# Optimization experiments

Measured on AMD Instinct MI355X. Metric: run time of the kernel, lower is better.

The kernel has to match this reference:

```python
import jax, jax.numpy as jnp
import numpy as np

NUM_USERS = 100000
NUM_ITEMS = 50000
N = NUM_USERS + NUM_ITEMS
E = 3000000
DIM = 64


def setup_inputs() -> dict:
    key = jax.random.key(0)
    ks = jax.random.split(key, 8)
    emb_users = 0.01 * jax.random.normal(ks[0], (NUM_USERS, DIM), dtype=jnp.float32)
    emb_items = 0.01 * jax.random.normal(ks[1], (NUM_ITEMS, DIM), dtype=jnp.float32)
    # GCNConv linear weights (bias separate, as in PyG: lin(bias=False) + bias param)
    s = 1.0 / np.sqrt(DIM)
    W1 = jax.random.uniform(ks[2], (DIM, DIM), jnp.float32, -s, s)
    b1 = jnp.zeros((DIM,), jnp.float32)
    W2 = jax.random.uniform(ks[3], (DIM, DIM), jnp.float32, -s, s)
    b2 = jnp.zeros((DIM,), jnp.float32)
    edge_index = jax.random.randint(ks[4], (2, E), 0, N, dtype=jnp.int64)
    edge_weight = jax.random.uniform(ks[5], (E,), jnp.float32)
    return {"emb_users": emb_users, "emb_items": emb_items,
            "W1": W1, "b1": b1, "W2": W2, "b2": b2,
            "edge_index": edge_index, "edge_weight": edge_weight}


def _gcn_conv(x, W, b, row, col):
    """PyG GCNConv with add_self_loops=True, improved=False, unit edge weights.
    out[i] = sum_{j->i} d_j^-1/2 d_i^-1/2 (x_j W) + d_i^-1 (x_i W) + b
    where d includes the self-loop (+1).
    """
    n = x.shape[0]
    xw = x @ W                                           # [N, D]
    deg = jax.ops.segment_sum(jnp.ones_like(row, dtype=x.dtype), col,
                              num_segments=n) + 1.0      # in-degree + self-loop
    dinv = jax.lax.rsqrt(deg)                            # [N]
    coef = dinv[row] * dinv[col]                         # [E]
    msg = xw[row] * coef[:, None]                        # gather + scale  [E, D]
    out = jax.ops.segment_sum(msg, col, num_segments=n)  # scatter-add     [N, D]
    out = out + xw * (dinv * dinv)[:, None]              # self-loop term
    return out + b


def reference(emb_users, emb_items, W1, b1, W2, b2, edge_index, edge_weight):
    # edge_weight is accepted by forward() but never passed to the GCN convs
    row, col = edge_index[0], edge_index[1]
    emb = jnp.concatenate([emb_users, emb_items], axis=0)  # [N, D]
    embs = [emb]
    for W, b in ((W1, b1), (W2, b2)):
        emb = _gcn_conv(emb, W, b, row, col)
        embs.append(emb)
        emb = jax.nn.relu(emb)
    return jnp.stack(embs)  # [num_layers+1, N, D]
```

## Files before the change

### kernel.cpp

```cpp
#include <hip/hip_runtime.h>
#include <hip/hip_fp16.h>

#define DIM 64
#define BPN 1024
#define ECHUNK 8192
#define MAXNB 160

typedef _Float16 f16x8 __attribute__((ext_vector_type(8)));
typedef float f32x4 __attribute__((ext_vector_type(4)));


__global__ __launch_bounds__(1024) void bucket_count_kernel(
    const int* __restrict__ col, int* __restrict__ bucket_cnt, int E, int NB) {
  __shared__ int h[MAXNB];
  for (int t = threadIdx.x; t < NB; t += blockDim.x) h[t] = 0;
  __syncthreads();
  int base = blockIdx.x * ECHUNK;
  int end = min(base + ECHUNK, E);
  for (int e = base + (int)threadIdx.x; e < end; e += blockDim.x)
    atomicAdd(&h[col[e] >> 10], 1);
  __syncthreads();
  for (int t = threadIdx.x; t < NB; t += blockDim.x)
    if (h[t]) atomicAdd(&bucket_cnt[t], h[t]);
}

__global__ void bucket_scan_kernel(const int* __restrict__ bucket_cnt,
                                   int* __restrict__ bucket_base,
                                   int* __restrict__ bucket_cursor,
                                   int* __restrict__ off, int NB, int N, int E) {
  if (threadIdx.x == 0) {
    int s = 0;
    for (int b = 0; b < NB; b++) { bucket_base[b] = s; bucket_cursor[b] = s; s += bucket_cnt[b]; }
    bucket_base[NB] = s;
    off[N] = E;
  }
}

__global__ __launch_bounds__(1024) void bucket_scatter_kernel(
    const int* __restrict__ row, const int* __restrict__ col,
    int* __restrict__ bucket_cursor, int* __restrict__ packed, int E, int NB) {
  __shared__ int h[MAXNB];
  __shared__ int excl0[MAXNB];
  __shared__ int cur[MAXNB];
  __shared__ int gbase[MAXNB];
  __shared__ int staging[ECHUNK];
  __shared__ unsigned short map[ECHUNK];
  const int tid = threadIdx.x;
  for (int t = tid; t < NB; t += blockDim.x) h[t] = 0;
  __syncthreads();
  int base = blockIdx.x * ECHUNK;
  int end = min(base + ECHUNK, E);
  int total = end - base;
  for (int e = base + tid; e < end; e += blockDim.x)
    atomicAdd(&h[col[e] >> 10], 1);
  __syncthreads();
  if (tid == 0) {
    int s = 0;
    for (int b = 0; b < NB; b++) { excl0[b] = s; cur[b] = s; s += h[b]; }
  }
  __syncthreads();
  if (tid < NB) {
    if (h[tid] > 0) gbase[tid] = atomicAdd(&bucket_cursor[tid], h[tid]);
    int s = excl0[tid], c = h[tid];
    for (int j = 0; j < c; j++) map[s + j] = (unsigned short)tid;
  }
  __syncthreads();
  for (int e = base + tid; e < end; e += blockDim.x) {
    int c = col[e];
    int b = c >> 10;
    int pos = atomicAdd(&cur[b], 1);
    staging[pos] = ((c & (BPN - 1)) << 18) | row[e];
  }
  __syncthreads();
  for (int idx = tid; idx < total; idx += blockDim.x) {
    int b = map[idx];
    packed[gbase[b] + idx - excl0[b]] = staging[idx];
  }
}

__global__ __launch_bounds__(1024) void bucket_csr_kernel(
    const int* __restrict__ packed, const int* __restrict__ bucket_base,
    int* __restrict__ perm_row, int* __restrict__ off, float* __restrict__ dinv, int N) {
  __shared__ int nh[BPN];
  __shared__ int ncur[BPN];
  __shared__ int wsum[16];
  __shared__ int woff[16];
  const int b = blockIdx.x;
  const int tid = threadIdx.x;
  const int ebase = bucket_base[b];
  const int cnt = bucket_base[b + 1] - ebase;
  nh[tid] = 0;
  __syncthreads();
  for (int i = tid; i < cnt; i += 1024)
    atomicAdd(&nh[packed[ebase + i] >> 18], 1);
  __syncthreads();
  const int lane = tid & 63, wid = tid >> 6;
  int v = nh[tid], x = v;
#pragma unroll
  for (int d = 1; d < 64; d <<= 1) {
    int t = __shfl_up(x, d, 64);
    if (lane >= d) x += t;
  }
  if (lane == 63) wsum[wid] = x;
  __syncthreads();
  if (tid == 0) {
    int s = 0;
#pragma unroll
    for (int k = 0; k < 16; k++) { woff[k] = s; s += wsum[k]; }
  }
  __syncthreads();
  int excl = woff[wid] + x - v;
  ncur[tid] = excl;
  int node = b * BPN + tid;
  if (node < N) {
    off[node] = ebase + excl;
    dinv[node] = rsqrtf((float)v + 1.0f);
  }
  __syncthreads();
  for (int i = tid; i < cnt; i += 1024) {
    int p = packed[ebase + i];
    int local = p >> 18;
    int pos = atomicAdd(&ncur[local], 1);
    perm_row[ebase + pos] = p & 0x3FFFF;
  }
}

__global__ __launch_bounds__(256) void xw_mfma_kernel(
    const float* __restrict__ xa, const float* __restrict__ xb,
    const float* __restrict__ W, float* __restrict__ out0,
    __half* __restrict__ xwh, int NU, int N, int do_relu) {
  __shared__ _Float16 Wt[64 * 72];
  for (int t = threadIdx.x; t < 4096; t += 256) {
    int k = t >> 6, n = t & 63;
    Wt[n * 72 + k] = (_Float16)W[t];
  }
  __syncthreads();
  const int lane = threadIdx.x & 63;
  const int wid = threadIdx.x >> 6;
  const int m = lane & 15;
  const int quad = lane >> 4;
  f16x8 bfrag[4][2];
#pragma unroll
  for (int c = 0; c < 4; c++)
#pragma unroll
    for (int s = 0; s < 2; s++)
      bfrag[c][s] = *(const f16x8*)&Wt[(c * 16 + m) * 72 + s * 32 + quad * 8];

  const int rbase = (blockIdx.x * 4 + wid) * 16;
  if (rbase >= N) return;
  const int r = rbase + m;
  const int rr = min(r, N - 1);
  const float* src = (xb == nullptr || rr < NU) ? xa + (size_t)rr * DIM
                                                : xb + (size_t)(rr - NU) * DIM;
  f16x8 afrag[2];
#pragma unroll
  for (int s = 0; s < 2; s++) {
    float4 u0 = *(const float4*)(src + s * 32 + quad * 8);
    float4 u1 = *(const float4*)(src + s * 32 + quad * 8 + 4);
    if (out0 != nullptr && r < N) {
      float4* o = (float4*)(out0 + (size_t)r * DIM);
      o[s * 8 + quad * 2] = u0;
      o[s * 8 + quad * 2 + 1] = u1;
    }
    if (do_relu) {
      u0.x = fmaxf(u0.x, 0.f); u0.y = fmaxf(u0.y, 0.f);
      u0.z = fmaxf(u0.z, 0.f); u0.w = fmaxf(u0.w, 0.f);
      u1.x = fmaxf(u1.x, 0.f); u1.y = fmaxf(u1.y, 0.f);
      u1.z = fmaxf(u1.z, 0.f); u1.w = fmaxf(u1.w, 0.f);
    }
    afrag[s][0] = (_Float16)u0.x; afrag[s][1] = (_Float16)u0.y;
    afrag[s][2] = (_Float16)u0.z; afrag[s][3] = (_Float16)u0.w;
    afrag[s][4] = (_Float16)u1.x; afrag[s][5] = (_Float16)u1.y;
    afrag[s][6] = (_Float16)u1.z; afrag[s][7] = (_Float16)u1.w;
  }
  f32x4 acc[4];
#pragma unroll
  for (int c = 0; c < 4; c++) {
    acc[c] = (f32x4){0.f, 0.f, 0.f, 0.f};
    acc[c] = __builtin_amdgcn_mfma_f32_16x16x32_f16(afrag[0], bfrag[c][0], acc[c], 0, 0, 0);
    acc[c] = __builtin_amdgcn_mfma_f32_16x16x32_f16(afrag[1], bfrag[c][1], acc[c], 0, 0, 0);
  }
#pragma unroll
  for (int reg = 0; reg < 4; reg++) {
    int orow = rbase + quad * 4 + reg;
    if (orow < N) {
      __half* dst = xwh + (size_t)orow * DIM + m;
#pragma unroll
      for (int c = 0; c < 4; c++)
        dst[c * 16] = __float2half(acc[c][reg]);
    }
  }
}

__global__ void aggregate_kernel(const __half* __restrict__ xwh, const int* __restrict__ off,
                                 const int* __restrict__ perm_row, const float* __restrict__ dinv,
                                 const float* __restrict__ b, float* __restrict__ out, int n) {
  const int lane = threadIdx.x & 63;
  const int i = blockIdx.x * (blockDim.x >> 6) + (threadIdx.x >> 6);
  if (i >= n) return;
  const int esel = lane >> 3;
  const int j = lane & 7;
  const float di = dinv[i];
  float acc[8];
#pragma unroll
  for (int q = 0; q < 8; q++) acc[q] = 0.0f;
  if (esel == 0) {
    float4 f = ((const float4*)xwh)[(size_t)i * 8 + j];
    const __half2* h = (const __half2*)&f;
    float w = di * di;
#pragma unroll
    for (int q = 0; q < 4; q++) {
      float2 p = __half22float2(h[q]);
      acc[2 * q] = p.x * w;
      acc[2 * q + 1] = p.y * w;
    }
  }
  int s0 = off[i], s1 = off[i + 1];
  for (int s = s0; s < s1; s += 64) {
    int m = s1 - s;
    if (m > 64) m = 64;
    int myr = 0;
    float myc = 0.0f;
    if (lane < m) {
      myr = perm_row[s + lane];
      myc = dinv[myr] * di;
    }
    for (int k = 0; k < m; k += 8) {
      int kk = k + esel;
      int r = __shfl(myr, kk, 64);
      float c = __shfl(myc, kk, 64);
      float4 f = ((const float4*)xwh)[(size_t)r * 8 + j];
      const __half2* h = (const __half2*)&f;
#pragma unroll
      for (int q = 0; q < 4; q++) {
        float2 p = __half22float2(h[q]);
        acc[2 * q] += c * p.x;
        acc[2 * q + 1] += c * p.y;
      }
    }
  }
#pragma unroll
  for (int q = 0; q < 8; q++) {
    acc[q] += __shfl_xor(acc[q], 8, 64);
    acc[q] += __shfl_xor(acc[q], 16, 64);
    acc[q] += __shfl_xor(acc[q], 32, 64);
  }
  if (esel == 0) {
    float4 b0 = ((const float4*)b)[2 * j];
    float4 b1 = ((const float4*)b)[2 * j + 1];
    float4* orow = (float4*)(out + (size_t)i * DIM);
    orow[2 * j] = make_float4(acc[0] + b0.x, acc[1] + b0.y, acc[2] + b0.z, acc[3] + b0.w);
    orow[2 * j + 1] = make_float4(acc[4] + b1.x, acc[5] + b1.y, acc[6] + b1.z, acc[7] + b1.w);
  }
}

extern "C" void kernel_launch(void* const* d_in, const int* in_sizes, int n_in,
                              void* d_out, int out_size, void* d_ws, size_t ws_size,
                              hipStream_t stream) {
  const float* emb_users = (const float*)d_in[0];
  const float* emb_items = (const float*)d_in[1];
  const float* W1 = (const float*)d_in[2];
  const float* b1 = (const float*)d_in[3];
  const float* W2 = (const float*)d_in[4];
  const float* b2 = (const float*)d_in[5];
  const int* edge_index = (const int*)d_in[6];

  const int NU = in_sizes[0] / DIM;
  const int NI = in_sizes[1] / DIM;
  const int N = NU + NI;
  const int E = in_sizes[6] / 2;
  const int NB = (N + BPN - 1) / BPN;
  const int* row = edge_index;
  const int* col = edge_index + E;

  float* out = (float*)d_out;

  char* ws = (char*)d_ws;
  size_t o = 0;
  auto alloc = [&](size_t bytes) -> void* {
    o = (o + 255) & ~(size_t)255;
    void* p = ws + o;
    o += bytes;
    return p;
  };
  int* bucket_cnt    = (int*)alloc((size_t)NB * 4);
  int* bucket_base   = (int*)alloc((size_t)(NB + 1) * 4);
  int* bucket_cursor = (int*)alloc((size_t)NB * 4);
  int* off           = (int*)alloc((size_t)(N + 1) * 4);
  float* dinv        = (float*)alloc((size_t)N * 4);
  int* perm_row      = (int*)alloc((size_t)E * 4);
  __half* xwh        = (__half*)alloc((size_t)N * DIM * 2);
  int* packed        = (int*)xwh;
  (void)ws_size;

  const int nbE = (E + ECHUNK - 1) / ECHUNK;

  hipMemsetAsync(bucket_cnt, 0, (size_t)NB * 4, stream);
  bucket_count_kernel<<<nbE, 1024, 0, stream>>>(col, bucket_cnt, E, NB);
  bucket_scan_kernel<<<1, 64, 0, stream>>>(bucket_cnt, bucket_base, bucket_cursor, off, NB, N, E);
  bucket_scatter_kernel<<<nbE, 1024, 0, stream>>>(row, col, bucket_cursor, packed, E, NB);
  bucket_csr_kernel<<<NB, 1024, 0, stream>>>(packed, bucket_base, perm_row, off, dinv, N);

  const int TB = 256;
  const int gr = (N + 3) / 4;
  const int gx = (N + 63) / 64;

  xw_mfma_kernel<<<gx, TB, 0, stream>>>(emb_users, emb_items, W1, out, xwh, NU, N, 0);
  aggregate_kernel<<<gr, TB, 0, stream>>>((const __half*)xwh, off, perm_row, dinv, b1,
                                          out + (size_t)N * DIM, N);

  xw_mfma_kernel<<<gx, TB, 0, stream>>>(out + (size_t)N * DIM, nullptr, W2, nullptr, xwh, N, N, 1);
  aggregate_kernel<<<gr, TB, 0, stream>>>((const __half*)xwh, off, perm_row, dinv, b2,
                                          out + (size_t)2 * N * DIM, N);
}
```

Measured before the change: 414.1 us.

## Precompute per-edge source dinv, factor out target dinv, prefetch gathers

Stores each CSR edge as an (row, dinv[row]) pair, filled by a new edge_coef kernel, so the aggregation no longer does a dependent random dinv lookup per edge in both layers. The target-side dinv is factored out of the per-edge coefficient and applied once at output. The inner gather loop is software-pipelined so the next row's half-precision features load while the current ones accumulate. In exchange the edge array doubles in size and an extra kernel pass over all edges is added.

```diff
diff --git a/kernel.cpp b/kernel.cpp
--- a/kernel.cpp
+++ b/kernel.cpp
@@ -80,7 +80,7 @@
 
 __global__ __launch_bounds__(1024) void bucket_csr_kernel(
     const int* __restrict__ packed, const int* __restrict__ bucket_base,
-    int* __restrict__ perm_row, int* __restrict__ off, float* __restrict__ dinv, int N) {
+    int2* __restrict__ edata, int* __restrict__ off, float* __restrict__ dinv, int N) {
   __shared__ int nh[BPN];
   __shared__ int ncur[BPN];
   __shared__ int wsum[16];
@@ -117,12 +117,21 @@
     dinv[node] = rsqrtf((float)v + 1.0f);
   }
   __syncthreads();
+  int* edx = (int*)edata;
   for (int i = tid; i < cnt; i += 1024) {
     int p = packed[ebase + i];
     int local = p >> 18;
     int pos = atomicAdd(&ncur[local], 1);
-    perm_row[ebase + pos] = p & 0x3FFFF;
-  }
+    edx[(size_t)(ebase + pos) * 2] = p & 0x3FFFF;
+  }
+}
+
+__global__ __launch_bounds__(256) void edge_coef_kernel(
+    int2* __restrict__ edata, const float* __restrict__ dinv, int E) {
+  int e = blockIdx.x * 256 + threadIdx.x;
+  if (e >= E) return;
+  int r = ((const int*)edata)[(size_t)e * 2];
+  edata[e] = make_int2(r, __float_as_int(dinv[r]));
 }
 
 __global__ __launch_bounds__(256) void xw_mfma_kernel(
@@ -193,7 +202,7 @@
 }
 
 __global__ void aggregate_kernel(const __half* __restrict__ xwh, const int* __restrict__ off,
-                                 const int* __restrict__ perm_row, const float* __restrict__ dinv,
+                                 const int2* __restrict__ edata, const float* __restrict__ dinv,
                                  const float* __restrict__ b, float* __restrict__ out, int n) {
   const int lane = threadIdx.x & 63;
   const int i = blockIdx.x * (blockDim.x >> 6) + (threadIdx.x >> 6);
@@ -207,12 +216,11 @@
   if (esel == 0) {
     float4 f = ((const float4*)xwh)[(size_t)i * 8 + j];
     const __half2* h = (const __half2*)&f;
-    float w = di * di;
 #pragma unroll
     for (int q = 0; q < 4; q++) {
       float2 p = __half22float2(h[q]);
-      acc[2 * q] = p.x * w;
-      acc[2 * q + 1] = p.y * w;
+      acc[2 * q] = di * p.x;
+      acc[2 * q + 1] = di * p.y;
     }
   }
   int s0 = off[i], s1 = off[i + 1];
@@ -222,21 +230,33 @@
     int myr = 0;
     float myc = 0.0f;
     if (lane < m) {
-      myr = perm_row[s + lane];
-      myc = dinv[myr] * di;
-    }
-    for (int k = 0; k < m; k += 8) {
-      int kk = k + esel;
-      int r = __shfl(myr, kk, 64);
-      float c = __shfl(myc, kk, 64);
-      float4 f = ((const float4*)xwh)[(size_t)r * 8 + j];
-      const __half2* h = (const __half2*)&f;
+      int2 v = edata[s + lane];
+      myr = v.x;
+      myc = __int_as_float(v.y);
+    }
+    int r0 = __shfl(myr, esel, 64);
+    float c0 = __shfl(myc, esel, 64);
+    float4 f0 = ((const float4*)xwh)[(size_t)r0 * 8 + j];
+    for (int k = 8; k < m; k += 8) {
+      int r1 = __shfl(myr, k + esel, 64);
+      float c1 = __shfl(myc, k + esel, 64);
+      float4 f1 = ((const float4*)xwh)[(size_t)r1 * 8 + j];
+      const __half2* h0 = (const __half2*)&f0;
 #pragma unroll
       for (int q = 0; q < 4; q++) {
-        float2 p = __half22float2(h[q]);
-        acc[2 * q] += c * p.x;
-        acc[2 * q + 1] += c * p.y;
+        float2 p = __half22float2(h0[q]);
+        acc[2 * q] += c0 * p.x;
+        acc[2 * q + 1] += c0 * p.y;
       }
+      f0 = f1;
+      c0 = c1;
+    }
+    const __half2* h0 = (const __half2*)&f0;
+#pragma unroll
+    for (int q = 0; q < 4; q++) {
+      float2 p = __half22float2(h0[q]);
+      acc[2 * q] += c0 * p.x;
+      acc[2 * q + 1] += c0 * p.y;
     }
   }
 #pragma unroll
@@ -249,8 +269,10 @@
     float4 b0 = ((const float4*)b)[2 * j];
     float4 b1 = ((const float4*)b)[2 * j + 1];
     float4* orow = (float4*)(out + (size_t)i * DIM);
-    orow[2 * j] = make_float4(acc[0] + b0.x, acc[1] + b0.y, acc[2] + b0.z, acc[3] + b0.w);
-    orow[2 * j + 1] = make_float4(acc[4] + b1.x, acc[5] + b1.y, acc[6] + b1.z, acc[7] + b1.w);
+    orow[2 * j] = make_float4(di * acc[0] + b0.x, di * acc[1] + b0.y,
+                              di * acc[2] + b0.z, di * acc[3] + b0.w);
+    orow[2 * j + 1] = make_float4(di * acc[4] + b1.x, di * acc[5] + b1.y,
+                                  di * acc[6] + b1.z, di * acc[7] + b1.w);
   }
 }
 
@@ -288,7 +310,7 @@
   int* bucket_cursor = (int*)alloc((size_t)NB * 4);
   int* off           = (int*)alloc((size_t)(N + 1) * 4);
   float* dinv        = (float*)alloc((size_t)N * 4);
-  int* perm_row      = (int*)alloc((size_t)E * 4);
+  int2* edata        = (int2*)alloc((size_t)E * 8);
   __half* xwh        = (__half*)alloc((size_t)N * DIM * 2);
   int* packed        = (int*)xwh;
   (void)ws_size;
@@ -299,17 +321,18 @@
   bucket_count_kernel<<<nbE, 1024, 0, stream>>>(col, bucket_cnt, E, NB);
   bucket_scan_kernel<<<1, 64, 0, stream>>>(bucket_cnt, bucket_base, bucket_cursor, off, NB, N, E);
   bucket_scatter_kernel<<<nbE, 1024, 0, stream>>>(row, col, bucket_cursor, packed, E, NB);
-  bucket_csr_kernel<<<NB, 1024, 0, stream>>>(packed, bucket_base, perm_row, off, dinv, N);
+  bucket_csr_kernel<<<NB, 1024, 0, stream>>>(packed, bucket_base, edata, off, dinv, N);
+  edge_coef_kernel<<<(E + 255) / 256, 256, 0, stream>>>(edata, dinv, E);
 
   const int TB = 256;
   const int gr = (N + 3) / 4;
   const int gx = (N + 63) / 64;
 
   xw_mfma_kernel<<<gx, TB, 0, stream>>>(emb_users, emb_items, W1, out, xwh, NU, N, 0);
-  aggregate_kernel<<<gr, TB, 0, stream>>>((const __half*)xwh, off, perm_row, dinv, b1,
+  aggregate_kernel<<<gr, TB, 0, stream>>>((const __half*)xwh, off, edata, dinv, b1,
                                           out + (size_t)N * DIM, N);
 
   xw_mfma_kernel<<<gx, TB, 0, stream>>>(out + (size_t)N * DIM, nullptr, W2, nullptr, xwh, N, N, 1);
-  aggregate_kernel<<<gr, TB, 0, stream>>>((const __half*)xwh, off, perm_row, dinv, b2,
+  aggregate_kernel<<<gr, TB, 0, stream>>>((const __half*)xwh, off, edata, dinv, b2,
                                           out + (size_t)2 * N * DIM, N);
 }
```

Measured after the change: 425.3 us. 2.7% more time.
